# Kernel tuning notes

Hardware: AMD Instinct MI355X
Metric: run time of the kernel (lower is better)

## Reference

```python
import jax, jax.numpy as jnp
import numpy as np

B, CIN, N = 4, 128, 4096
CKEY, COUT = 64, 128

def setup_inputs() -> dict:
    key = jax.random.key(0)
    k1, k2, k3, k4 = jax.random.split(key, 4)
    x = jax.random.normal(k1, (B, CIN, N), dtype=jnp.float32)
    # Conv1d(kernel_size=1, bias=False) weights as [out, in] matrices
    Wq = jax.random.normal(k2, (CKEY, CIN), dtype=jnp.float32) * (1.0 / np.sqrt(CIN))
    Wk = jax.random.normal(k3, (CKEY, CIN), dtype=jnp.float32) * (1.0 / np.sqrt(CIN))
    Wv = jax.random.normal(k4, (COUT, CIN), dtype=jnp.float32) * (1.0 / np.sqrt(CIN))
    return {"x": x, "Wq": Wq, "Wk": Wk, "Wv": Wv}

def reference(x, Wq, Wk, Wv):
    # 1x1 conv projections: [B, C, N] -> [B, C', N]
    Q = jnp.einsum('ki,bin->bkn', Wq, x)   # [B, CKEY, N]
    K = jnp.einsum('ki,bin->bkn', Wk, x)   # [B, CKEY, N]
    V = jnp.einsum('oi,bin->bon', Wv, x)   # [B, COUT, N]
    # A = softmax(Q^T K) over last dim -- NOTE: no 1/sqrt(d) scaling, as in original
    scores = jnp.einsum('bkn,bkm->bnm', Q, K)     # [B, N, N]
    A = jax.nn.softmax(scores, axis=2)
    # out = (A @ V^T)^T -> [B, COUT, N]
    out = jnp.einsum('bnm,bom->bon', A, V)
    return out
```

## Files before the change

kernel.cpp:

```cpp
#include <hip/hip_runtime.h>
#include <hip/hip_bf16.h>

#define NN    4096
#define BB    4
#define CIN_  128
#define COUT_ 128

typedef __attribute__((ext_vector_type(8))) short bf16x8;
typedef __attribute__((ext_vector_type(4))) short bf16x4;
typedef __attribute__((ext_vector_type(4))) float f32x4;
typedef __attribute__((ext_vector_type(2))) int   i32x2;

#define MFMA16 __builtin_amdgcn_mfma_f32_16x16x32_bf16
#define SWK(row, g) ((((row) << 6)) + ((((g) ^ ((row) & 7))) << 3))

__device__ __forceinline__ float bf2f(short s) {
    union { unsigned int u; float f; } c; c.u = ((unsigned int)(unsigned short)s) << 16; return c.f;
}
__device__ __forceinline__ short f2bf(float f) {
    union { float f; unsigned int u; } c; c.f = f;
    unsigned int r = c.u + 0x7fffu + ((c.u >> 16) & 1u);
    return (short)(r >> 16);
}
__device__ __forceinline__ float fexp2(float x) {
#if __has_builtin(__builtin_amdgcn_exp2f)
    return __builtin_amdgcn_exp2f(x);
#else
    return exp2f(x);
#endif
}
__device__ __forceinline__ unsigned int pack_bf16(float a, float b) {
    union { float f; unsigned int u; } ca, cb; ca.f = a; cb.f = b;
    unsigned int ua = ca.u + 0x8000u, ub = cb.u + 0x8000u;
#if __has_builtin(__builtin_amdgcn_perm)
    return __builtin_amdgcn_perm(ub, ua, 0x07060302u);
#else
    return (ua >> 16) | (ub & 0xffff0000u);
#endif
}
__device__ __forceinline__ void gll16(const short* g, short* l) {
    __builtin_amdgcn_global_load_lds(
        (const __attribute__((address_space(1))) void*)g,
        (__attribute__((address_space(3))) void*)l, 16, 0, 0);
}

__global__ __launch_bounds__(1024) void proj_kernel(const float* __restrict__ x,
                                                    const float* __restrict__ Wq,
                                                    const float* __restrict__ Wk,
                                                    const float* __restrict__ Wv,
                                                    short* __restrict__ Qh, short* __restrict__ Ql,
                                                    short* __restrict__ Kh, short* __restrict__ Kl,
                                                    short* __restrict__ Vb) {
    __shared__ __align__(16) short xsh[16 * 64 * 8];
    __shared__ __align__(16) short xsl[16 * 64 * 8];

    int tid  = threadIdx.x;
    int b    = blockIdx.y;
    int gn0  = blockIdx.x * 64;
    int wave = tid >> 6;
    int lane = tid & 63;
    int quad = lane >> 4;
    int l15  = lane & 15;

    const float* xb = x + (size_t)b * CIN_ * NN + gn0;
    {
        int c = tid >> 6, n = tid & 63;
        bf16x8 h8, l8;
#pragma unroll
        for (int j = 0; j < 8; ++j) {
            float f = xb[(c * 8 + j) * NN + n];
            short h = f2bf(f);
            h8[j] = h;
            l8[j] = f2bf(f - bf2f(h));
        }
        *(bf16x8*)(xsh + (c * 64 + n) * 8) = h8;
        *(bf16x8*)(xsl + (c * 64 + n) * 8) = l8;
    }
    __syncthreads();

    int rg = wave;

    const float* wrow;
    float scale = 1.0f;
    if (rg < 4)      { wrow = Wq + (rg * 16 + l15) * CIN_; scale = 1.4426950408889634f; }
    else if (rg < 8) { wrow = Wk + ((rg - 4) * 16 + l15) * CIN_; }
    else             { wrow = Wv + ((rg - 8) * 16 + l15) * CIN_; }

    bf16x8 wh[4], wl[4];
#pragma unroll
    for (int kc = 0; kc < 4; ++kc) {
        const float* wp = wrow + kc * 32 + quad * 8;
#pragma unroll
        for (int j = 0; j < 8; ++j) {
            float w = wp[j] * scale;
            short h = f2bf(w);
            wh[kc][j] = h;
            wl[kc][j] = f2bf(w - bf2f(h));
        }
    }

    f32x4 acc[4];
#pragma unroll
    for (int ct = 0; ct < 4; ++ct) acc[ct] = (f32x4){0.f, 0.f, 0.f, 0.f};

#pragma unroll
    for (int kc = 0; kc < 4; ++kc) {
#pragma unroll
        for (int ct = 0; ct < 4; ++ct) {
            bf16x8 xh = *(const bf16x8*)(xsh + (((kc * 4 + quad) * 64) + ct * 16 + l15) * 8);
            bf16x8 xl = *(const bf16x8*)(xsl + (((kc * 4 + quad) * 64) + ct * 16 + l15) * 8);
            acc[ct] = MFMA16(wh[kc], xh, acc[ct], 0, 0, 0);
            acc[ct] = MFMA16(wh[kc], xl, acc[ct], 0, 0, 0);
            acc[ct] = MFMA16(wl[kc], xh, acc[ct], 0, 0, 0);
        }
    }

    if (rg < 8) {
        short* H = (rg < 4) ? Qh : Kh;
        short* L = (rg < 4) ? Ql : Kl;
        int rb    = (rg < 4) ? rg : (rg - 4);
        int chunk = rb * 2 + (quad >> 1);
        int sub   = (quad & 1) * 4;
#pragma unroll
        for (int ct = 0; ct < 4; ++ct) {
            int n = gn0 + ct * 16 + l15;
            bf16x4 h4, l4;
#pragma unroll
            for (int r = 0; r < 4; ++r) {
                float f = acc[ct][r];
                short h = f2bf(f);
                h4[r] = h;
                l4[r] = f2bf(f - bf2f(h));
            }
            *(bf16x4*)(H + (((b * 8 + chunk) * NN) + n) * 8 + sub) = h4;
            *(bf16x4*)(L + (((b * 8 + chunk) * NN) + n) * 8 + sub) = l4;
        }
    } else {
        int o0 = rg * 16 + quad * 4 - 128;
#pragma unroll
        for (int ct = 0; ct < 4; ++ct) {
            int n = gn0 + ct * 16 + l15;
#pragma unroll
            for (int r = 0; r < 4; ++r)
                Vb[((size_t)(b * COUT_ + o0 + r)) * NN + n] = f2bf(acc[ct][r]);
        }
    }
}

__global__ __launch_bounds__(256, 2) void flash_kernel(const short* __restrict__ Qh,
                                                       const short* __restrict__ Ql,
                                                       const short* __restrict__ Kh,
                                                       const short* __restrict__ Kl,
                                                       const short* __restrict__ Vb,
                                                       float* __restrict__ outp,
                                                       short* __restrict__ opart,
                                                       float* __restrict__ lsum,
                                                       int S, int direct) {
    __shared__ __align__(16) short VT[2 * 128 * 64];
    __shared__ __align__(16) short PW[4 * 32 * 64];
    __shared__ __align__(16) short KT[2 * 8192];

    int tid  = threadIdx.x;
    int bx   = blockIdx.x;
    int b    = bx / S;
    int s    = bx - b * S;
    int qt   = blockIdx.y;
    int wave = tid >> 6;
    int lane = tid & 63;
    int quad = lane >> 4;
    int l15  = lane & 15;
    int l8   = lane >> 3;
    int l7   = lane & 7;

    int nq0 = qt * 128 + wave * 32 + l15;
    bf16x8 qh0[2], qh1[2], ql0[2], ql1[2];
#pragma unroll
    for (int u = 0; u < 2; ++u) {
        int nq = nq0 + u * 16;
        qh0[u] = *(const bf16x8*)(Qh + (((b * 8 + quad)     * NN) + nq) * 8);
        qh1[u] = *(const bf16x8*)(Qh + (((b * 8 + 4 + quad) * NN) + nq) * 8);
        ql0[u] = *(const bf16x8*)(Ql + (((b * 8 + quad)     * NN) + nq) * 8);
        ql1[u] = *(const bf16x8*)(Ql + (((b * 8 + 4 + quad) * NN) + nq) * 8);
    }

    f32x4 O[2][8];
#pragma unroll
    for (int u = 0; u < 2; ++u)
#pragma unroll
        for (int f = 0; f < 8; ++f) O[u][f] = (f32x4){0.f, 0.f, 0.f, 0.f};
    float lp[2] = {0.f, 0.f};

    short* pwb = PW + wave * 2048;

    int KPS   = NN / S;
    int kb    = s * KPS;
    int iters = KPS / 64;

    const short* KhB = Kh + (size_t)b * 8 * NN * 8;
    const short* KlB = Kl + (size_t)b * 8 * NN * 8;
    const short* VbB = Vb + (size_t)b * COUT_ * NN;

    const short* vsrc = VbB + (size_t)(wave * 8 + l8) * NN + (l7 ^ l8) * 8;
    int vdst = wave * 512;

    const short* ksrc0 = KhB + ((size_t)(wave)     * NN + lane) * 8;
    const short* ksrc1 = KhB + ((size_t)(4 + wave) * NN + lane) * 8;
    const short* ksrc2 = KlB + ((size_t)(wave)     * NN + lane) * 8;
    const short* ksrc3 = KlB + ((size_t)(4 + wave) * NN + lane) * 8;
    int kdstw = wave * 512;

    {
        short* kd = KT + kdstw;
        gll16(ksrc0 + kb * 8, kd);
        gll16(ksrc1 + kb * 8, kd + 2048);
        gll16(ksrc2 + kb * 8, kd + 4096);
        gll16(ksrc3 + kb * 8, kd + 6144);
#pragma unroll
        for (int j = 0; j < 4; ++j)
            gll16(vsrc + (size_t)j * 32 * NN + kb, VT + vdst + j * 2048);
    }

    int cur = 0;
    for (int it = 0; it < iters; ++it) {
        __syncthreads();

        if (it + 1 < iters) {
            int nb = kb + 64;
            short* kd = KT + (cur ^ 1) * 8192 + kdstw;
            gll16(ksrc0 + nb * 8, kd);
            gll16(ksrc1 + nb * 8, kd + 2048);
            gll16(ksrc2 + nb * 8, kd + 4096);
            gll16(ksrc3 + nb * 8, kd + 6144);
            short* vb1 = VT + ((cur ^ 1) << 13) + vdst;
#pragma unroll
            for (int j = 0; j < 4; ++j)
                gll16(vsrc + (size_t)j * 32 * NN + nb, vb1 + j * 2048);
        }

        const short* kt = KT + cur * 8192;
        bf16x8 kh0[4], kh1[4], kl0[4], kl1[4];
#pragma unroll
        for (int f = 0; f < 4; ++f) {
            int ro = f * 16 + l15;
            kh0[f] = *(const bf16x8*)(kt + (quad * 64 + ro) * 8);
            kh1[f] = *(const bf16x8*)(kt + ((4 + quad) * 64 + ro) * 8);
            kl0[f] = *(const bf16x8*)(kt + 4096 + (quad * 64 + ro) * 8);
            kl1[f] = *(const bf16x8*)(kt + 4096 + ((4 + quad) * 64 + ro) * 8);
        }

        f32x4 sA[2][4];
        __builtin_amdgcn_s_setprio(1);
#pragma unroll
        for (int f = 0; f < 4; ++f) {
#pragma unroll
            for (int u = 0; u < 2; ++u) {
                f32x4 acc = (f32x4){0.f, 0.f, 0.f, 0.f};
                acc = MFMA16(kh0[f], qh0[u], acc, 0, 0, 0);
                acc = MFMA16(kh1[f], qh1[u], acc, 0, 0, 0);
                acc = MFMA16(kl0[f], qh0[u], acc, 0, 0, 0);
                acc = MFMA16(kl1[f], qh1[u], acc, 0, 0, 0);
                acc = MFMA16(kh0[f], ql0[u], acc, 0, 0, 0);
                acc = MFMA16(kh1[f], ql1[u], acc, 0, 0, 0);
                sA[u][f] = acc;
            }
        }
        __builtin_amdgcn_s_setprio(0);

#pragma unroll
        for (int u = 0; u < 2; ++u) {
            int row = u * 16 + l15;
#pragma unroll
            for (int f = 0; f < 4; ++f) {
                float p0 = fexp2(sA[u][f][0]);
                float p1 = fexp2(sA[u][f][1]);
                float p2 = fexp2(sA[u][f][2]);
                float p3 = fexp2(sA[u][f][3]);
                lp[u] += (p0 + p1) + (p2 + p3);
                unsigned int w0 = pack_bf16(p0, p1);
                unsigned int w1 = pack_bf16(p2, p3);
                *(i32x2*)(pwb + SWK(row, f * 2 + (quad >> 1)) + (quad & 1) * 4) =
                    (i32x2){(int)w0, (int)w1};
            }
        }

        {
            const short* vt = VT + (cur << 13);
            __builtin_amdgcn_s_setprio(1);
#pragma unroll
            for (int g = 0; g < 2; ++g) {
                bf16x8 pb0 = *(const bf16x8*)(pwb + SWK(l15,      g * 4 + quad));
                bf16x8 pb1 = *(const bf16x8*)(pwb + SWK(16 + l15, g * 4 + quad));
#pragma unroll
                for (int f8 = 0; f8 < 8; ++f8) {
                    bf16x8 vA = *(const bf16x8*)(vt + SWK(f8 * 16 + l15, g * 4 + quad));
                    O[0][f8] = MFMA16(vA, pb0, O[0][f8], 0, 0, 0);
                    O[1][f8] = MFMA16(vA, pb1, O[1][f8], 0, 0, 0);
                }
            }
            __builtin_amdgcn_s_setprio(0);
        }
        cur ^= 1;
        kb += 64;
    }

#pragma unroll
    for (int u = 0; u < 2; ++u) {
        lp[u] += __shfl_xor(lp[u], 16, 64);
        lp[u] += __shfl_xor(lp[u], 32, 64);
    }

#pragma unroll
    for (int u = 0; u < 2; ++u) {
        int n = nq0 + u * 16;
        if (direct) {
            float inv = 1.f / lp[u];
#pragma unroll
            for (int f8 = 0; f8 < 8; ++f8)
#pragma unroll
                for (int r = 0; r < 4; ++r) {
                    int o = f8 * 16 + quad * 4 + r;
                    outp[((size_t)(b * COUT_ + o)) * NN + n] = O[u][f8][r] * inv;
                }
        } else {
#pragma unroll
            for (int f8 = 0; f8 < 8; ++f8)
#pragma unroll
                for (int r = 0; r < 4; ++r) {
                    int o = f8 * 16 + quad * 4 + r;
                    opart[((size_t)((b * S + s) * COUT_ + o)) * NN + n] = f2bf(O[u][f8][r]);
                }
            if (quad == 0) lsum[(b * S + s) * NN + n] = lp[u];
        }
    }
}

__global__ __launch_bounds__(256, 4) void merge_kernel(const short* __restrict__ Opart,
                                                       const float* __restrict__ lsum,
                                                       float* __restrict__ out, int S) {
    int idx = blockIdx.x * 256 + threadIdx.x;
    int n0  = (idx & (NN / 4 - 1)) * 4;
    int rest = idx >> 10;
    int o = rest & (COUT_ - 1);
    int b = rest >> 7;

    f32x4 den = (f32x4){0.f, 0.f, 0.f, 0.f};
    f32x4 acc = (f32x4){0.f, 0.f, 0.f, 0.f};
    for (int s = 0; s < S; ++s) {
        f32x4 l  = *(const f32x4*)(lsum + (b * S + s) * NN + n0);
        bf16x4 ov = *(const bf16x4*)(Opart + ((size_t)((b * S + s) * COUT_ + o)) * NN + n0);
#pragma unroll
        for (int j = 0; j < 4; ++j) {
            den[j] += l[j];
            acc[j] += bf2f(ov[j]);
        }
    }
    f32x4 res;
#pragma unroll
    for (int j = 0; j < 4; ++j) res[j] = acc[j] / den[j];
    *(f32x4*)(out + ((size_t)(b * COUT_ + o)) * NN + n0) = res;
}

extern "C" void kernel_launch(void* const* d_in, const int* in_sizes, int n_in,
                              void* d_out, int out_size, void* d_ws, size_t ws_size,
                              hipStream_t stream) {
    const float* x  = (const float*)d_in[0];
    const float* Wq = (const float*)d_in[1];
    const float* Wk = (const float*)d_in[2];
    const float* Wv = (const float*)d_in[3];

    char* ws = (char*)d_ws;
    short* Qh = (short*)ws;
    short* Ql = Qh + 1048576;
    short* Kh = Ql + 1048576;
    short* Kl = Kh + 1048576;
    short* Vb = Kl + 1048576;
    size_t base = 4ull * 2097152 + 4194304;
    const size_t MLSZ  = (size_t)BB * NN * 4;
    const size_t OPB   = (size_t)BB * COUT_ * NN * 2;

    int S;
    if (ws_size >= base + 4 * (MLSZ + OPB)) S = 4;
    else                                    S = 1;
    int direct = (S == 1);

    float* lsum  = (float*)(ws + base);
    short* Opart = (short*)(ws + base + (size_t)S * MLSZ);

    proj_kernel<<<dim3(NN / 64, BB), 1024, 0, stream>>>(x, Wq, Wk, Wv, Qh, Ql, Kh, Kl, Vb);
    flash_kernel<<<dim3(BB * S, NN / 128), 256, 0, stream>>>(
        Qh, Ql, Kh, Kl, Vb, (float*)d_out, Opart, lsum, S, direct);
    if (!direct)
        merge_kernel<<<BB * COUT_ * NN / 4 / 256, 256, 0, stream>>>(Opart, lsum, (float*)d_out, S);
}
```

Before: 122.5 us.

## Fuse split-K merge into flash kernel via last-block atomic counter

Replaces the separate merge kernel with an in-kernel reduction. Each split block bumps an atomic counter per (batch, query tile), and the last arriving block sums the partial outputs and normalizers and writes the final result. This removes one kernel launch and the round trip between kernels, but it adds a memset launch, threadfences, and a serialized tail in which the last block reads all partials.

Result: slower. 230.0 us (+87.7%).

```diff
diff --git a/kernel.cpp b/kernel.cpp
--- a/kernel.cpp
+++ b/kernel.cpp
@@ -155,10 +155,12 @@
                                                        float* __restrict__ outp,
                                                        short* __restrict__ opart,
                                                        float* __restrict__ lsum,
+                                                       int* __restrict__ cnt,
                                                        int S, int direct) {
     __shared__ __align__(16) short VT[2 * 128 * 64];
     __shared__ __align__(16) short PW[4 * 32 * 64];
     __shared__ __align__(16) short KT[2 * 8192];
+    __shared__ int lastflag;
 
     int tid  = threadIdx.x;
     int bx   = blockIdx.x;
@@ -332,32 +334,38 @@
             if (quad == 0) lsum[(b * S + s) * NN + n] = lp[u];
         }
     }
-}
-
-__global__ __launch_bounds__(256, 4) void merge_kernel(const short* __restrict__ Opart,
-                                                       const float* __restrict__ lsum,
-                                                       float* __restrict__ out, int S) {
-    int idx = blockIdx.x * 256 + threadIdx.x;
-    int n0  = (idx & (NN / 4 - 1)) * 4;
-    int rest = idx >> 10;
-    int o = rest & (COUT_ - 1);
-    int b = rest >> 7;
-
-    f32x4 den = (f32x4){0.f, 0.f, 0.f, 0.f};
-    f32x4 acc = (f32x4){0.f, 0.f, 0.f, 0.f};
-    for (int s = 0; s < S; ++s) {
-        f32x4 l  = *(const f32x4*)(lsum + (b * S + s) * NN + n0);
-        bf16x4 ov = *(const bf16x4*)(Opart + ((size_t)((b * S + s) * COUT_ + o)) * NN + n0);
-#pragma unroll
-        for (int j = 0; j < 4; ++j) {
-            den[j] += l[j];
-            acc[j] += bf2f(ov[j]);
-        }
-    }
-    f32x4 res;
-#pragma unroll
-    for (int j = 0; j < 4; ++j) res[j] = acc[j] / den[j];
-    *(f32x4*)(out + ((size_t)(b * COUT_ + o)) * NN + n0) = res;
+
+    if (!direct) {
+        __syncthreads();
+        if (tid == 0) {
+            __threadfence();
+            int old = atomicAdd(&cnt[b * (NN / 128) + qt], 1);
+            lastflag = (old == S - 1);
+        }
+        __syncthreads();
+        if (lastflag) {
+            __threadfence();
+            for (int t = tid; t < COUT_ * 32; t += 256) {
+                int o  = t >> 5;
+                int n0 = qt * 128 + (t & 31) * 4;
+                f32x4 den = (f32x4){0.f, 0.f, 0.f, 0.f};
+                f32x4 acc = (f32x4){0.f, 0.f, 0.f, 0.f};
+                for (int s2 = 0; s2 < S; ++s2) {
+                    f32x4 l   = *(const f32x4*)(lsum + (b * S + s2) * NN + n0);
+                    bf16x4 ov = *(const bf16x4*)(opart + ((size_t)((b * S + s2) * COUT_ + o)) * NN + n0);
+#pragma unroll
+                    for (int j = 0; j < 4; ++j) {
+                        den[j] += l[j];
+                        acc[j] += bf2f(ov[j]);
+                    }
+                }
+                f32x4 res;
+#pragma unroll
+                for (int j = 0; j < 4; ++j) res[j] = acc[j] / den[j];
+                *(f32x4*)(outp + ((size_t)(b * COUT_ + o)) * NN + n0) = res;
+            }
+        }
+    }
 }
 
 extern "C" void kernel_launch(void* const* d_in, const int* in_sizes, int n_in,
@@ -377,18 +385,20 @@
     size_t base = 4ull * 2097152 + 4194304;
     const size_t MLSZ  = (size_t)BB * NN * 4;
     const size_t OPB   = (size_t)BB * COUT_ * NN * 2;
+    const size_t CNTSZ = (size_t)BB * (NN / 128) * sizeof(int);
 
     int S;
-    if (ws_size >= base + 4 * (MLSZ + OPB)) S = 4;
-    else                                    S = 1;
+    if (ws_size >= base + 4 * (MLSZ + OPB) + CNTSZ) S = 4;
+    else                                            S = 1;
     int direct = (S == 1);
 
     float* lsum  = (float*)(ws + base);
     short* Opart = (short*)(ws + base + (size_t)S * MLSZ);
+    int*   cnt   = (int*)(ws + base + (size_t)S * (MLSZ + OPB));
 
     proj_kernel<<<dim3(NN / 64, BB), 1024, 0, stream>>>(x, Wq, Wk, Wv, Qh, Ql, Kh, Kl, Vb);
+    if (!direct)
+        hipMemsetAsync(cnt, 0, CNTSZ, stream);
     flash_kernel<<<dim3(BB * S, NN / 128), 256, 0, stream>>>(
-        Qh, Ql, Kh, Kl, Vb, (float*)d_out, Opart, lsum, S, direct);
-    if (!direct)
-        merge_kernel<<<BB * COUT_ * NN / 4 / 256, 256, 0, stream>>>(Opart, lsum, (float*)d_out, S);
-}
+        Qh, Ql, Kh, Kl, Vb, (float*)d_out, Opart, lsum, cnt, S, direct);
+}
```
